# Performance work log

Hardware: AMD Instinct MI355X
Metric: run time of the kernel (lower is better)

## Reference

```python
import jax, jax.numpy as jnp
import numpy as np


def setup_inputs() -> dict:
    key = jax.random.key(0)
    ks = jax.random.split(key, 5)
    B, S, D, E, H = 8, 4096, 512, 4, 64
    x = jax.random.normal(ks[0], (B, S, D), dtype=jnp.float32)
    router_w = jax.random.normal(ks[1], (D, E), dtype=jnp.float32) * 0.02
    router_b = jnp.zeros((E,), dtype=jnp.float32)
    w1 = jax.random.normal(ks[2], (E, D, H), dtype=jnp.float32) * 0.02
    b1 = jnp.zeros((E, H), dtype=jnp.float32)
    w2 = jax.random.normal(ks[3], (E, H, D), dtype=jnp.float32) * 0.02
    b2 = jnp.zeros((E, D), dtype=jnp.float32)
    return {"x": x, "router_w": router_w, "router_b": router_b,
            "w1": w1, "b1": b1, "w2": w2, "b2": b2}


def reference(x, router_w, router_b, w1, b1, w2, b2):
    # Router: softmax over experts. weights: [B, S, E]
    weights = jax.nn.softmax(jnp.einsum('bsd,de->bse', x, router_w) + router_b, axis=-1)
    # All experts run densely on every token (batched over the E axis).
    # h: [B, S, E, H]; TF Dense(activation='gelu') uses exact (non-tanh) gelu.
    h = jax.nn.gelu(jnp.einsum('bsd,edh->bseh', x, w1) + b1, approximate=False)
    # expert outputs: [B, S, E, D]; Dropout is identity at inference.
    expert_out = jnp.einsum('bseh,ehd->bsed', h, w2) + b2
    # weighted sum over experts -> [B, S, D]
    return jnp.sum(expert_out * weights[..., None], axis=2)
```

## Files before the change

kernel.cpp:

```cpp
#include <hip/hip_runtime.h>
#include <hip/hip_bf16.h>
#include <math.h>


typedef short v8s __attribute__((ext_vector_type(8)));
typedef float v4f __attribute__((ext_vector_type(4)));

#define XS 520
#define HS 296

__device__ __forceinline__ unsigned short f2bf(float f) {
    unsigned int u = __builtin_bit_cast(unsigned int, f);
    u += 0x7fffu + ((u >> 16) & 1u);
    return (unsigned short)(u >> 16);
}

__global__ void moe_prep(const float* __restrict__ w1,
                         const float* __restrict__ w2,
                         const float* __restrict__ b2,
                         const float* __restrict__ rw,
                         unsigned short* __restrict__ w1p,
                         unsigned short* __restrict__ w2p,
                         unsigned short* __restrict__ rp) {
    int idx = blockIdx.x * 256 + threadIdx.x;
    if (idx < 131072) {
        int block = idx >> 9, within = idx & 511;
        int kb = block >> 4, cb = block & 15;
        int n = within >> 5, kl = within & 31;
        int k = kb * 32 + kl;
        int col = cb * 16 + n;
        int e = col >> 6, h = col & 63;
        w1p[idx] = f2bf(w1[(e * 512 + k) * 64 + h]);
    } else if (idx < 131072 + 147456) {
        int op = idx - 131072;
        int block = op >> 9, within = op & 511;
        int kb = block >> 5, cb = block & 31;
        int n = within >> 5, kl = within & 31;
        int k = kb * 32 + kl;
        int d = cb * 16 + n;
        float v = 0.f;
        if (k < 256) {
            int e = k >> 6, h = k & 63;
            v = w2[(e * 64 + h) * 512 + d];
        } else if (k < 260) {
            v = b2[(k - 256) * 512 + d];
        }
        w2p[op] = f2bf(v);
    } else if (idx < 131072 + 147456 + 8192) {
        int op = idx - (131072 + 147456);
        int kb = op >> 9, within = op & 511;
        int n = within >> 5, kl = within & 31;
        int k = kb * 32 + kl;
        float v = (n < 4) ? rw[k * 4 + n] : 0.f;
        rp[op] = f2bf(v);
    }
}

__global__ __launch_bounds__(512, 4)
void moe_main(const float* __restrict__ x,
              const float* __restrict__ rb,
              const float* __restrict__ b1,
              const unsigned short* __restrict__ w1p,
              const unsigned short* __restrict__ w2p,
              const unsigned short* __restrict__ rp,
              float* __restrict__ out) {
    __shared__ __align__(16) unsigned short lx[64 * XS];
    __shared__ float lw[64 * 4];

    const int tid  = threadIdx.x;
    const int lane = tid & 63, wv = tid >> 6;
    const int lr = lane & 15, lq = lane >> 4;
    const long t0 = (long)blockIdx.x * 64;

    const float4* xt = (const float4*)(x + t0 * 512);
    #pragma unroll
    for (int it = 0; it < 16; ++it) {
        int F = it * 512 + tid;
        int row = F >> 7, c4 = F & 127;
        float4 v = xt[F];
        unsigned int p0 = (unsigned int)f2bf(v.x) | ((unsigned int)f2bf(v.y) << 16);
        unsigned int p1 = (unsigned int)f2bf(v.z) | ((unsigned int)f2bf(v.w) << 16);
        *(uint2*)&lx[row * XS + c4 * 4] = make_uint2(p0, p1);
    }
    __syncthreads();

    v4f acc1[4][2];
    v4f accR;
    accR[0] = accR[1] = accR[2] = accR[3] = 0.f;
    #pragma unroll
    for (int mt = 0; mt < 4; ++mt)
        #pragma unroll
        for (int nt = 0; nt < 2; ++nt)
            acc1[mt][nt][0] = acc1[mt][nt][1] = acc1[mt][nt][2] = acc1[mt][nt][3] = 0.f;

    for (int kb = 0; kb < 16; ++kb) {
        v8s a[4], b[2];
        #pragma unroll
        for (int mt = 0; mt < 4; ++mt)
            a[mt] = *(const v8s*)(const void*)&lx[(16 * mt + lr) * XS + kb * 32 + lq * 8];
        #pragma unroll
        for (int nt = 0; nt < 2; ++nt)
            b[nt] = *(const v8s*)(const void*)&w1p[(size_t)(kb * 16 + 2 * wv + nt) * 512 + lr * 32 + lq * 8];
        if (wv < 4) {
            v8s ar = *(const v8s*)(const void*)&lx[(16 * wv + lr) * XS + kb * 32 + lq * 8];
            v8s br = *(const v8s*)(const void*)&rp[kb * 512 + lr * 32 + lq * 8];
            accR = __builtin_amdgcn_mfma_f32_16x16x32_bf16(ar, br, accR, 0, 0, 0);
        }
        #pragma unroll
        for (int mt = 0; mt < 4; ++mt)
            #pragma unroll
            for (int nt = 0; nt < 2; ++nt)
                acc1[mt][nt] = __builtin_amdgcn_mfma_f32_16x16x32_bf16(a[mt], b[nt], acc1[mt][nt], 0, 0, 0);
    }

    if (wv < 4) {
        float rbv = rb[lane & 3];
        #pragma unroll
        for (int r = 0; r < 4; ++r) {
            float v = accR[r] + rbv;
            float m = fmaxf(v, __shfl_xor(v, 1));
            m = fmaxf(m, __shfl_xor(m, 2));
            float e = expf(v - m);
            float s = e + __shfl_xor(e, 1);
            s += __shfl_xor(s, 2);
            if (lr < 4)
                lw[(16 * wv + lq * 4 + r) * 4 + lr] = e / s;
        }
    }

    __syncthreads();

    {
        const int e = wv >> 1;
        float b1v[2];
        #pragma unroll
        for (int nt = 0; nt < 2; ++nt)
            b1v[nt] = b1[e * 64 + 32 * (wv & 1) + 16 * nt + lr];
        #pragma unroll
        for (int mt = 0; mt < 4; ++mt) {
            #pragma unroll
            for (int r = 0; r < 4; ++r) {
                int row = 16 * mt + lq * 4 + r;
                float wt = lw[row * 4 + e];
                #pragma unroll
                for (int nt = 0; nt < 2; ++nt) {
                    float v = acc1[mt][nt][r] + b1v[nt];
                    float g = 0.5f * v * (1.f + erff(v * 0.70710678118f)) * wt;
                    lx[row * HS + 32 * wv + 16 * nt + lr] = f2bf(g);
                }
            }
        }
        if (tid < 256) {
            int r = tid >> 2, e4 = tid & 3;
            lx[r * HS + 256 + e4] = f2bf(lw[r * 4 + e4]);
            #pragma unroll
            for (int i = 0; i < 7; ++i)
                lx[r * HS + 260 + e4 + 4 * i] = 0;
        }
    }
    __syncthreads();

    v4f acc2[4][4];
    #pragma unroll
    for (int mt = 0; mt < 4; ++mt)
        #pragma unroll
        for (int nt = 0; nt < 4; ++nt)
            acc2[mt][nt][0] = acc2[mt][nt][1] = acc2[mt][nt][2] = acc2[mt][nt][3] = 0.f;

    for (int kb = 0; kb < 9; ++kb) {
        v8s a[4], b[4];
        #pragma unroll
        for (int mt = 0; mt < 4; ++mt)
            a[mt] = *(const v8s*)(const void*)&lx[(16 * mt + lr) * HS + kb * 32 + lq * 8];
        #pragma unroll
        for (int nt = 0; nt < 4; ++nt)
            b[nt] = *(const v8s*)(const void*)&w2p[(size_t)(kb * 32 + 4 * wv + nt) * 512 + lr * 32 + lq * 8];
        #pragma unroll
        for (int mt = 0; mt < 4; ++mt)
            #pragma unroll
            for (int nt = 0; nt < 4; ++nt)
                acc2[mt][nt] = __builtin_amdgcn_mfma_f32_16x16x32_bf16(a[mt], b[nt], acc2[mt][nt], 0, 0, 0);
    }

    float* ot = out + t0 * 512;
    #pragma unroll
    for (int mt = 0; mt < 4; ++mt)
        #pragma unroll
        for (int nt = 0; nt < 4; ++nt)
            #pragma unroll
            for (int r = 0; r < 4; ++r) {
                int row = 16 * mt + lq * 4 + r;
                int col = 64 * wv + 16 * nt + lr;
                ot[row * 512 + col] = acc2[mt][nt][r];
            }
}

extern "C" void kernel_launch(void* const* d_in, const int* in_sizes, int n_in,
                              void* d_out, int out_size, void* d_ws, size_t ws_size,
                              hipStream_t stream) {
    const float* x  = (const float*)d_in[0];
    const float* rw = (const float*)d_in[1];
    const float* rb = (const float*)d_in[2];
    const float* w1 = (const float*)d_in[3];
    const float* b1 = (const float*)d_in[4];
    const float* w2 = (const float*)d_in[5];
    const float* b2 = (const float*)d_in[6];

    unsigned short* w1p = (unsigned short*)d_ws;
    unsigned short* w2p = w1p + 131072;
    unsigned short* rp  = w2p + 147456;

    moe_prep<<<1120, 256, 0, stream>>>(w1, w2, b2, rw, w1p, w2p, rp);
    moe_main<<<512, 512, 0, stream>>>(x, rb, b1, w1p, w2p, rp, (float*)d_out);
}
```

Before: 156.5 us.

## Split fused MoE kernel into two GEMM kernels with global hidden buffer

Splits the single fused kernel into one kernel computing the router softmax and gated GELU hidden activations, which are written to a global bf16 buffer, and a second kernel doing the output GEMM over twice as many blocks. The first kernel now reads x straight from global memory into registers instead of staging it through LDS, and uses fewer threads per block with more accumulator tiles per wave. Exact erf and expf are replaced by a polynomial erf approximation and fast exp. This gives up fusion, adding an HBM round trip for the hidden buffer and an extra launch, in exchange for lower LDS use, higher occupancy and more parallelism in the second GEMM.

```diff
diff --git a/kernel.cpp b/kernel.cpp
--- a/kernel.cpp
+++ b/kernel.cpp
@@ -5,14 +5,24 @@
 
 typedef short v8s __attribute__((ext_vector_type(8)));
 typedef float v4f __attribute__((ext_vector_type(4)));
-
-#define XS 520
-#define HS 296
 
 __device__ __forceinline__ unsigned short f2bf(float f) {
     unsigned int u = __builtin_bit_cast(unsigned int, f);
     u += 0x7fffu + ((u >> 16) & 1u);
     return (unsigned short)(u >> 16);
+}
+__device__ __forceinline__ unsigned int pk2(float lo, float hi) {
+    return (unsigned int)f2bf(lo) | ((unsigned int)f2bf(hi) << 16);
+}
+__device__ __forceinline__ float gelu_fast(float v) {
+    float s  = v * 0.70710678118f;
+    float xa = fabsf(s);
+    float t  = 1.0f / (1.0f + 0.3275911f * xa);
+    float poly = t * (0.254829592f + t * (-0.284496736f + t * (1.421413741f +
+                 t * (-1.453152027f + t * 1.061405429f))));
+    float er = 1.0f - poly * __expf(-xa * xa);
+    er = copysignf(er, s);
+    return 0.5f * v * (1.0f + er);
 }
 
 __global__ void moe_prep(const float* __restrict__ w1,
@@ -56,15 +66,13 @@
     }
 }
 
-__global__ __launch_bounds__(512, 4)
-void moe_main(const float* __restrict__ x,
-              const float* __restrict__ rb,
-              const float* __restrict__ b1,
-              const unsigned short* __restrict__ w1p,
-              const unsigned short* __restrict__ w2p,
-              const unsigned short* __restrict__ rp,
-              float* __restrict__ out) {
-    __shared__ __align__(16) unsigned short lx[64 * XS];
+__global__ __launch_bounds__(256, 3)
+void moe_g1(const float* __restrict__ x,
+            const float* __restrict__ rb,
+            const float* __restrict__ b1,
+            const unsigned short* __restrict__ w1p,
+            const unsigned short* __restrict__ rp,
+            unsigned short* __restrict__ hbuf) {
     __shared__ float lw[64 * 4];
 
     const int tid  = threadIdx.x;
@@ -72,117 +80,114 @@
     const int lr = lane & 15, lq = lane >> 4;
     const long t0 = (long)blockIdx.x * 64;
 
-    const float4* xt = (const float4*)(x + t0 * 512);
-    #pragma unroll
-    for (int it = 0; it < 16; ++it) {
-        int F = it * 512 + tid;
-        int row = F >> 7, c4 = F & 127;
-        float4 v = xt[F];
-        unsigned int p0 = (unsigned int)f2bf(v.x) | ((unsigned int)f2bf(v.y) << 16);
-        unsigned int p1 = (unsigned int)f2bf(v.z) | ((unsigned int)f2bf(v.w) << 16);
-        *(uint2*)&lx[row * XS + c4 * 4] = make_uint2(p0, p1);
-    }
-    __syncthreads();
-
-    v4f acc1[4][2];
+    v4f acc1[4][4];
     v4f accR;
     accR[0] = accR[1] = accR[2] = accR[3] = 0.f;
     #pragma unroll
     for (int mt = 0; mt < 4; ++mt)
         #pragma unroll
-        for (int nt = 0; nt < 2; ++nt)
+        for (int nt = 0; nt < 4; ++nt)
             acc1[mt][nt][0] = acc1[mt][nt][1] = acc1[mt][nt][2] = acc1[mt][nt][3] = 0.f;
 
+    #pragma unroll 2
     for (int kb = 0; kb < 16; ++kb) {
-        v8s a[4], b[2];
+        v8s a[4], b[4];
+        #pragma unroll
+        for (int mt = 0; mt < 4; ++mt) {
+            const float4* p = (const float4*)(x + (size_t)(t0 + 16 * mt + lr) * 512 + kb * 32 + lq * 8);
+            float4 u0 = p[0], u1 = p[1];
+            uint4 c = make_uint4(pk2(u0.x, u0.y), pk2(u0.z, u0.w),
+                                 pk2(u1.x, u1.y), pk2(u1.z, u1.w));
+            a[mt] = __builtin_bit_cast(v8s, c);
+        }
+        #pragma unroll
+        for (int nt = 0; nt < 4; ++nt)
+            b[nt] = *(const v8s*)(const void*)&w1p[(size_t)(kb * 16 + wv * 4 + nt) * 512 + lr * 32 + lq * 8];
+        v8s br = *(const v8s*)(const void*)&rp[kb * 512 + lr * 32 + lq * 8];
+        accR = __builtin_amdgcn_mfma_f32_16x16x32_bf16(a[wv], br, accR, 0, 0, 0);
         #pragma unroll
         for (int mt = 0; mt < 4; ++mt)
-            a[mt] = *(const v8s*)(const void*)&lx[(16 * mt + lr) * XS + kb * 32 + lq * 8];
-        #pragma unroll
-        for (int nt = 0; nt < 2; ++nt)
-            b[nt] = *(const v8s*)(const void*)&w1p[(size_t)(kb * 16 + 2 * wv + nt) * 512 + lr * 32 + lq * 8];
-        if (wv < 4) {
-            v8s ar = *(const v8s*)(const void*)&lx[(16 * wv + lr) * XS + kb * 32 + lq * 8];
-            v8s br = *(const v8s*)(const void*)&rp[kb * 512 + lr * 32 + lq * 8];
-            accR = __builtin_amdgcn_mfma_f32_16x16x32_bf16(ar, br, accR, 0, 0, 0);
-        }
-        #pragma unroll
-        for (int mt = 0; mt < 4; ++mt)
-            #pragma unroll
-            for (int nt = 0; nt < 2; ++nt)
+            #pragma unroll
+            for (int nt = 0; nt < 4; ++nt)
                 acc1[mt][nt] = __builtin_amdgcn_mfma_f32_16x16x32_bf16(a[mt], b[nt], acc1[mt][nt], 0, 0, 0);
     }
 
-    if (wv < 4) {
+    {
         float rbv = rb[lane & 3];
         #pragma unroll
         for (int r = 0; r < 4; ++r) {
             float v = accR[r] + rbv;
             float m = fmaxf(v, __shfl_xor(v, 1));
             m = fmaxf(m, __shfl_xor(m, 2));
-            float e = expf(v - m);
+            float e = __expf(v - m);
             float s = e + __shfl_xor(e, 1);
             s += __shfl_xor(s, 2);
             if (lr < 4)
                 lw[(16 * wv + lq * 4 + r) * 4 + lr] = e / s;
         }
     }
-
     __syncthreads();
 
     {
-        const int e = wv >> 1;
-        float b1v[2];
-        #pragma unroll
-        for (int nt = 0; nt < 2; ++nt)
-            b1v[nt] = b1[e * 64 + 32 * (wv & 1) + 16 * nt + lr];
+        float b1v[4];
+        #pragma unroll
+        for (int nt = 0; nt < 4; ++nt) b1v[nt] = b1[wv * 64 + nt * 16 + lr];
         #pragma unroll
         for (int mt = 0; mt < 4; ++mt) {
             #pragma unroll
             for (int r = 0; r < 4; ++r) {
                 int row = 16 * mt + lq * 4 + r;
-                float wt = lw[row * 4 + e];
+                float wt = lw[row * 4 + wv];
                 #pragma unroll
-                for (int nt = 0; nt < 2; ++nt) {
+                for (int nt = 0; nt < 4; ++nt) {
                     float v = acc1[mt][nt][r] + b1v[nt];
-                    float g = 0.5f * v * (1.f + erff(v * 0.70710678118f)) * wt;
-                    lx[row * HS + 32 * wv + 16 * nt + lr] = f2bf(g);
+                    float g = gelu_fast(v) * wt;
+                    hbuf[(size_t)(t0 + row) * 288 + wv * 64 + nt * 16 + lr] = f2bf(g);
                 }
             }
         }
-        if (tid < 256) {
-            int r = tid >> 2, e4 = tid & 3;
-            lx[r * HS + 256 + e4] = f2bf(lw[r * 4 + e4]);
-            #pragma unroll
-            for (int i = 0; i < 7; ++i)
-                lx[r * HS + 260 + e4 + 4 * i] = 0;
-        }
-    }
-    __syncthreads();
-
-    v4f acc2[4][4];
+        int rr = tid >> 2, e4 = tid & 3;
+        hbuf[(size_t)(t0 + rr) * 288 + 256 + e4] = f2bf(lw[rr * 4 + e4]);
+        #pragma unroll
+        for (int i = 0; i < 7; ++i)
+            hbuf[(size_t)(t0 + rr) * 288 + 260 + e4 * 7 + i] = 0;
+    }
+}
+
+__global__ __launch_bounds__(256, 3)
+void moe_g2(const unsigned short* __restrict__ hbuf,
+            const unsigned short* __restrict__ w2p,
+            float* __restrict__ out) {
+    const int tid  = threadIdx.x;
+    const int lane = tid & 63, wv = tid >> 6;
+    const int lr = lane & 15, lq = lane >> 4;
+    const long t0 = (long)(blockIdx.x >> 1) * 64;
+    const int nh = blockIdx.x & 1;
+    const int cb0 = nh * 16 + wv * 4;
+
+    v4f acc[4][4];
     #pragma unroll
     for (int mt = 0; mt < 4; ++mt)
         #pragma unroll
         for (int nt = 0; nt < 4; ++nt)
-            acc2[mt][nt][0] = acc2[mt][nt][1] = acc2[mt][nt][2] = acc2[mt][nt][3] = 0.f;
-
+            acc[mt][nt][0] = acc[mt][nt][1] = acc[mt][nt][2] = acc[mt][nt][3] = 0.f;
+
+    #pragma unroll 3
     for (int kb = 0; kb < 9; ++kb) {
         v8s a[4], b[4];
         #pragma unroll
         for (int mt = 0; mt < 4; ++mt)
-            a[mt] = *(const v8s*)(const void*)&lx[(16 * mt + lr) * HS + kb * 32 + lq * 8];
-        #pragma unroll
-        for (int nt = 0; nt < 4; ++nt)
-            b[nt] = *(const v8s*)(const void*)&w2p[(size_t)(kb * 32 + 4 * wv + nt) * 512 + lr * 32 + lq * 8];
+            a[mt] = *(const v8s*)(const void*)&hbuf[(size_t)(t0 + 16 * mt + lr) * 288 + kb * 32 + lq * 8];
+        #pragma unroll
+        for (int nt = 0; nt < 4; ++nt)
+            b[nt] = *(const v8s*)(const void*)&w2p[(size_t)(kb * 32 + cb0 + nt) * 512 + lr * 32 + lq * 8];
         #pragma unroll
         for (int mt = 0; mt < 4; ++mt)
             #pragma unroll
             for (int nt = 0; nt < 4; ++nt)
-                acc2[mt][nt] = __builtin_amdgcn_mfma_f32_16x16x32_bf16(a[mt], b[nt], acc2[mt][nt], 0, 0, 0);
-    }
-
-    float* ot = out + t0 * 512;
+                acc[mt][nt] = __builtin_amdgcn_mfma_f32_16x16x32_bf16(a[mt], b[nt], acc[mt][nt], 0, 0, 0);
+    }
+
     #pragma unroll
     for (int mt = 0; mt < 4; ++mt)
         #pragma unroll
@@ -190,8 +195,8 @@
             #pragma unroll
             for (int r = 0; r < 4; ++r) {
                 int row = 16 * mt + lq * 4 + r;
-                int col = 64 * wv + 16 * nt + lr;
-                ot[row * 512 + col] = acc2[mt][nt][r];
+                int col = nh * 256 + wv * 64 + 16 * nt + lr;
+                out[(size_t)(t0 + row) * 512 + col] = acc[mt][nt][r];
             }
 }
 
@@ -206,10 +211,12 @@
     const float* w2 = (const float*)d_in[5];
     const float* b2 = (const float*)d_in[6];
 
-    unsigned short* w1p = (unsigned short*)d_ws;
-    unsigned short* w2p = w1p + 131072;
-    unsigned short* rp  = w2p + 147456;
+    unsigned short* w1p  = (unsigned short*)d_ws;
+    unsigned short* w2p  = w1p + 131072;
+    unsigned short* rp   = w2p + 147456;
+    unsigned short* hbuf = rp + 8192;
 
     moe_prep<<<1120, 256, 0, stream>>>(w1, w2, b2, rw, w1p, w2p, rp);
-    moe_main<<<512, 512, 0, stream>>>(x, rb, b1, w1p, w2p, rp, (float*)d_out);
-}
+    moe_g1<<<512, 256, 0, stream>>>(x, rb, b1, w1p, rp, hbuf);
+    moe_g2<<<1024, 256, 0, stream>>>(hbuf, w2p, (float*)d_out);
+}
```

Result: slower. 210.8 us (+34.7%).

## Halve block to 4 waves, double-buffer weight loads, use fast GELU

Applied to the files above, without the earlier changes.

Shrinks the block from 8 to 4 waves so each wave covers one expert's full 64-column hidden slice and two 64-column output halves. Weight fragments from global memory are now double-buffered so the next k-step's loads overlap the current MFMAs. Exact erff is replaced by an Abramowitz-Stegun erf polynomial with __expf, and softmax also uses __expf. The cost is more register pressure per wave and fewer waves per block to hide latency, plus a small accuracy loss in GELU.

```diff
diff --git a/kernel.cpp b/kernel.cpp
--- a/kernel.cpp
+++ b/kernel.cpp
@@ -13,6 +13,15 @@
     unsigned int u = __builtin_bit_cast(unsigned int, f);
     u += 0x7fffu + ((u >> 16) & 1u);
     return (unsigned short)(u >> 16);
+}
+__device__ __forceinline__ float gelu_fast(float v) {
+    float s  = v * 0.70710678118f;
+    float xa = fabsf(s);
+    float t  = 1.0f / (1.0f + 0.3275911f * xa);
+    float poly = t * (0.254829592f + t * (-0.284496736f + t * (1.421413741f +
+                 t * (-1.453152027f + t * 1.061405429f))));
+    float er = copysignf(1.0f - poly * __expf(-xa * xa), s);
+    return 0.5f * v * (1.0f + er);
 }
 
 __global__ void moe_prep(const float* __restrict__ w1,
@@ -56,7 +65,7 @@
     }
 }
 
-__global__ __launch_bounds__(512, 4)
+__global__ __launch_bounds__(256, 2)
 void moe_main(const float* __restrict__ x,
               const float* __restrict__ rb,
               const float* __restrict__ b1,
@@ -74,8 +83,8 @@
 
     const float4* xt = (const float4*)(x + t0 * 512);
     #pragma unroll
-    for (int it = 0; it < 16; ++it) {
-        int F = it * 512 + tid;
+    for (int it = 0; it < 32; ++it) {
+        int F = it * 256 + tid;
         int row = F >> 7, c4 = F & 127;
         float4 v = xt[F];
         unsigned int p0 = (unsigned int)f2bf(v.x) | ((unsigned int)f2bf(v.y) << 16);
@@ -84,115 +93,161 @@
     }
     __syncthreads();
 
-    v4f acc1[4][2];
+    v4f acc1[4][4];
     v4f accR;
     accR[0] = accR[1] = accR[2] = accR[3] = 0.f;
     #pragma unroll
     for (int mt = 0; mt < 4; ++mt)
         #pragma unroll
-        for (int nt = 0; nt < 2; ++nt)
+        for (int nt = 0; nt < 4; ++nt)
             acc1[mt][nt][0] = acc1[mt][nt][1] = acc1[mt][nt][2] = acc1[mt][nt][3] = 0.f;
 
-    for (int kb = 0; kb < 16; ++kb) {
-        v8s a[4], b[2];
-        #pragma unroll
-        for (int mt = 0; mt < 4; ++mt)
-            a[mt] = *(const v8s*)(const void*)&lx[(16 * mt + lr) * XS + kb * 32 + lq * 8];
-        #pragma unroll
-        for (int nt = 0; nt < 2; ++nt)
-            b[nt] = *(const v8s*)(const void*)&w1p[(size_t)(kb * 16 + 2 * wv + nt) * 512 + lr * 32 + lq * 8];
-        if (wv < 4) {
-            v8s ar = *(const v8s*)(const void*)&lx[(16 * wv + lr) * XS + kb * 32 + lq * 8];
-            v8s br = *(const v8s*)(const void*)&rp[kb * 512 + lr * 32 + lq * 8];
-            accR = __builtin_amdgcn_mfma_f32_16x16x32_bf16(ar, br, accR, 0, 0, 0);
-        }
-        #pragma unroll
-        for (int mt = 0; mt < 4; ++mt)
-            #pragma unroll
-            for (int nt = 0; nt < 2; ++nt)
-                acc1[mt][nt] = __builtin_amdgcn_mfma_f32_16x16x32_bf16(a[mt], b[nt], acc1[mt][nt], 0, 0, 0);
-    }
-
-    if (wv < 4) {
+    const unsigned short* w1base = w1p + (size_t)(wv * 4) * 512 + lr * 32 + lq * 8;
+    const unsigned short* rpbase = rp + lr * 32 + lq * 8;
+
+    #define LDW1(B, BR, kb) do {                                                   \
+        _Pragma("unroll")                                                          \
+        for (int nt_ = 0; nt_ < 4; ++nt_)                                          \
+            B[nt_] = *(const v8s*)(const void*)&w1base[(size_t)((kb) * 16 + nt_) * 512]; \
+        BR = *(const v8s*)(const void*)&rpbase[(kb) * 512];                        \
+    } while (0)
+
+    #define MM1(B, BR, kb) do {                                                    \
+        v8s a_[4];                                                                 \
+        _Pragma("unroll")                                                          \
+        for (int mt_ = 0; mt_ < 4; ++mt_)                                          \
+            a_[mt_] = *(const v8s*)(const void*)&lx[(16 * mt_ + lr) * XS + (kb) * 32 + lq * 8]; \
+        v8s ar_ = *(const v8s*)(const void*)&lx[(16 * wv + lr) * XS + (kb) * 32 + lq * 8];      \
+        accR = __builtin_amdgcn_mfma_f32_16x16x32_bf16(ar_, BR, accR, 0, 0, 0);    \
+        _Pragma("unroll")                                                          \
+        for (int mt_ = 0; mt_ < 4; ++mt_)                                          \
+            _Pragma("unroll")                                                      \
+            for (int nt_ = 0; nt_ < 4; ++nt_)                                      \
+                acc1[mt_][nt_] = __builtin_amdgcn_mfma_f32_16x16x32_bf16(a_[mt_], B[nt_], acc1[mt_][nt_], 0, 0, 0); \
+    } while (0)
+
+    {
+        v8s b0[4], b1[4], br0, br1;
+        LDW1(b0, br0, 0);
+        #pragma unroll
+        for (int kp = 0; kp < 8; ++kp) {
+            LDW1(b1, br1, 2 * kp + 1);
+            MM1(b0, br0, 2 * kp);
+            if (kp < 7) LDW1(b0, br0, 2 * kp + 2);
+            MM1(b1, br1, 2 * kp + 1);
+        }
+    }
+
+    {
         float rbv = rb[lane & 3];
         #pragma unroll
         for (int r = 0; r < 4; ++r) {
             float v = accR[r] + rbv;
             float m = fmaxf(v, __shfl_xor(v, 1));
             m = fmaxf(m, __shfl_xor(m, 2));
-            float e = expf(v - m);
+            float e = __expf(v - m);
             float s = e + __shfl_xor(e, 1);
             s += __shfl_xor(s, 2);
             if (lr < 4)
                 lw[(16 * wv + lq * 4 + r) * 4 + lr] = e / s;
         }
     }
-
     __syncthreads();
 
+    const unsigned short* w2base = w2p + (size_t)(wv * 8) * 512 + lr * 32 + lq * 8;
+
+    v8s c0[4], c1[4];
+    #pragma unroll
+    for (int nt_ = 0; nt_ < 4; ++nt_)
+        c0[nt_] = *(const v8s*)(const void*)&w2base[(size_t)nt_ * 512];
+
     {
-        const int e = wv >> 1;
-        float b1v[2];
-        #pragma unroll
-        for (int nt = 0; nt < 2; ++nt)
-            b1v[nt] = b1[e * 64 + 32 * (wv & 1) + 16 * nt + lr];
+        float b1v[4];
+        #pragma unroll
+        for (int nt = 0; nt < 4; ++nt) b1v[nt] = b1[wv * 64 + nt * 16 + lr];
         #pragma unroll
         for (int mt = 0; mt < 4; ++mt) {
             #pragma unroll
             for (int r = 0; r < 4; ++r) {
                 int row = 16 * mt + lq * 4 + r;
-                float wt = lw[row * 4 + e];
+                float wt = lw[row * 4 + wv];
                 #pragma unroll
-                for (int nt = 0; nt < 2; ++nt) {
+                for (int nt = 0; nt < 4; ++nt) {
                     float v = acc1[mt][nt][r] + b1v[nt];
-                    float g = 0.5f * v * (1.f + erff(v * 0.70710678118f)) * wt;
-                    lx[row * HS + 32 * wv + 16 * nt + lr] = f2bf(g);
+                    float g = gelu_fast(v) * wt;
+                    lx[row * HS + wv * 64 + nt * 16 + lr] = f2bf(g);
                 }
             }
         }
-        if (tid < 256) {
-            int r = tid >> 2, e4 = tid & 3;
-            lx[r * HS + 256 + e4] = f2bf(lw[r * 4 + e4]);
-            #pragma unroll
-            for (int i = 0; i < 7; ++i)
-                lx[r * HS + 260 + e4 + 4 * i] = 0;
-        }
+        int r = tid >> 2, e = tid & 3;
+        lx[r * HS + 256 + e] = f2bf(lw[tid]);
+        #pragma unroll
+        for (int i = 0; i < 7; ++i)
+            lx[r * HS + 260 + e + 4 * i] = 0;
     }
     __syncthreads();
 
-    v4f acc2[4][4];
-    #pragma unroll
-    for (int mt = 0; mt < 4; ++mt)
-        #pragma unroll
-        for (int nt = 0; nt < 4; ++nt)
-            acc2[mt][nt][0] = acc2[mt][nt][1] = acc2[mt][nt][2] = acc2[mt][nt][3] = 0.f;
-
-    for (int kb = 0; kb < 9; ++kb) {
-        v8s a[4], b[4];
+    float* ot = out + t0 * 512;
+
+    #define LDW2(C, kb, h) do {                                                    \
+        _Pragma("unroll")                                                          \
+        for (int nt_ = 0; nt_ < 4; ++nt_)                                          \
+            C[nt_] = *(const v8s*)(const void*)&w2base[(size_t)((kb) * 32 + (h) * 4 + nt_) * 512]; \
+    } while (0)
+
+    #define MM2(C, kb) do {                                                        \
+        v8s a_[4];                                                                 \
+        _Pragma("unroll")                                                          \
+        for (int mt_ = 0; mt_ < 4; ++mt_)                                          \
+            a_[mt_] = *(const v8s*)(const void*)&lx[(16 * mt_ + lr) * HS + (kb) * 32 + lq * 8]; \
+        _Pragma("unroll")                                                          \
+        for (int mt_ = 0; mt_ < 4; ++mt_)                                          \
+            _Pragma("unroll")                                                      \
+            for (int nt_ = 0; nt_ < 4; ++nt_)                                      \
+                acc2[mt_][nt_] = __builtin_amdgcn_mfma_f32_16x16x32_bf16(a_[mt_], C[nt_], acc2[mt_][nt_], 0, 0, 0); \
+    } while (0)
+
+    #pragma unroll 1
+    for (int half = 0; half < 2; ++half) {
+        v4f acc2[4][4];
         #pragma unroll
         for (int mt = 0; mt < 4; ++mt)
-            a[mt] = *(const v8s*)(const void*)&lx[(16 * mt + lr) * HS + kb * 32 + lq * 8];
-        #pragma unroll
-        for (int nt = 0; nt < 4; ++nt)
-            b[nt] = *(const v8s*)(const void*)&w2p[(size_t)(kb * 32 + 4 * wv + nt) * 512 + lr * 32 + lq * 8];
+            #pragma unroll
+            for (int nt = 0; nt < 4; ++nt)
+                acc2[mt][nt][0] = acc2[mt][nt][1] = acc2[mt][nt][2] = acc2[mt][nt][3] = 0.f;
+
+        #pragma unroll
+        for (int kp = 0; kp < 4; ++kp) {
+            LDW2(c1, 2 * kp + 1, half);
+            MM2(c0, 2 * kp);
+            LDW2(c0, 2 * kp + 2, half);
+            MM2(c1, 2 * kp + 1);
+        }
+        if (half == 0) {
+            LDW2(c1, 0, 1);
+        }
+        MM2(c0, 8);
+
         #pragma unroll
         for (int mt = 0; mt < 4; ++mt)
             #pragma unroll
             for (int nt = 0; nt < 4; ++nt)
-                acc2[mt][nt] = __builtin_amdgcn_mfma_f32_16x16x32_bf16(a[mt], b[nt], acc2[mt][nt], 0, 0, 0);
-    }
-
-    float* ot = out + t0 * 512;
-    #pragma unroll
-    for (int mt = 0; mt < 4; ++mt)
-        #pragma unroll
-        for (int nt = 0; nt < 4; ++nt)
-            #pragma unroll
-            for (int r = 0; r < 4; ++r) {
-                int row = 16 * mt + lq * 4 + r;
-                int col = 64 * wv + 16 * nt + lr;
-                ot[row * 512 + col] = acc2[mt][nt][r];
-            }
+                #pragma unroll
+                for (int r = 0; r < 4; ++r) {
+                    int row = 16 * mt + lq * 4 + r;
+                    int col = 128 * wv + 64 * half + 16 * nt + lr;
+                    ot[row * 512 + col] = acc2[mt][nt][r];
+                }
+
+        if (half == 0) {
+            #pragma unroll
+            for (int nt_ = 0; nt_ < 4; ++nt_) c0[nt_] = c1[nt_];
+        }
+    }
+    #undef LDW1
+    #undef MM1
+    #undef LDW2
+    #undef MM2
 }
 
 extern "C" void kernel_launch(void* const* d_in, const int* in_sizes, int n_in,
@@ -211,5 +266,5 @@
     unsigned short* rp  = w2p + 147456;
 
     moe_prep<<<1120, 256, 0, stream>>>(w1, w2, b2, rw, w1p, w2p, rp);
-    moe_main<<<512, 512, 0, stream>>>(x, rb, b1, w1p, w2p, rp, (float*)d_out);
-}
+    moe_main<<<512, 256, 0, stream>>>(x, rb, b1, w1p, w2p, rp, (float*)d_out);
+}
```

New measurement: 150.1 us. 4.1% less time.

## Switch to 32x32x16 MFMA tiles with 4-wave blocks and fast GELU

Applied to the files above, without the earlier changes.

Replaces the 16x16x32 bf16 MFMA with 32x32x16 MFMA and repacks the weights in the prep kernel to match the new fragment layout. The main kernel drops from 8 waves to 4 per block, so each wave computes a larger 64x64 or 64x128 tile, and the router GEMM now runs on two waves. Exact erff in GELU is replaced by the Abramowitz-Stegun polynomial with __expf, and expf becomes __expf. The intent is better MFMA throughput and fewer B-fragment loads per FLOP, at the cost of fewer waves per block for hiding latency and slightly lower GELU accuracy.

```diff
diff --git a/kernel.cpp b/kernel.cpp
--- a/kernel.cpp
+++ b/kernel.cpp
@@ -3,8 +3,8 @@
 #include <math.h>
 
 
-typedef short v8s __attribute__((ext_vector_type(8)));
-typedef float v4f __attribute__((ext_vector_type(4)));
+typedef short v8s  __attribute__((ext_vector_type(8)));
+typedef float v16f __attribute__((ext_vector_type(16)));
 
 #define XS 520
 #define HS 296
@@ -13,6 +13,15 @@
     unsigned int u = __builtin_bit_cast(unsigned int, f);
     u += 0x7fffu + ((u >> 16) & 1u);
     return (unsigned short)(u >> 16);
+}
+__device__ __forceinline__ float gelu_fast(float v) {
+    float s  = v * 0.70710678118f;
+    float xa = fabsf(s);
+    float t  = 1.0f / (1.0f + 0.3275911f * xa);
+    float poly = t * (0.254829592f + t * (-0.284496736f + t * (1.421413741f +
+                 t * (-1.453152027f + t * 1.061405429f))));
+    float er = copysignf(1.0f - poly * __expf(-xa * xa), s);
+    return 0.5f * v * (1.0f + er);
 }
 
 __global__ void moe_prep(const float* __restrict__ w1,
@@ -25,19 +34,19 @@
     int idx = blockIdx.x * 256 + threadIdx.x;
     if (idx < 131072) {
         int block = idx >> 9, within = idx & 511;
-        int kb = block >> 4, cb = block & 15;
-        int n = within >> 5, kl = within & 31;
-        int k = kb * 32 + kl;
-        int col = cb * 16 + n;
+        int kstep = block >> 3, cb = block & 7;
+        int n = within >> 4, kl = within & 15;
+        int k = kstep * 16 + kl;
+        int col = cb * 32 + n;
         int e = col >> 6, h = col & 63;
         w1p[idx] = f2bf(w1[(e * 512 + k) * 64 + h]);
     } else if (idx < 131072 + 147456) {
         int op = idx - 131072;
         int block = op >> 9, within = op & 511;
-        int kb = block >> 5, cb = block & 31;
-        int n = within >> 5, kl = within & 31;
-        int k = kb * 32 + kl;
-        int d = cb * 16 + n;
+        int kstep = block >> 4, cb = block & 15;
+        int n = within >> 4, kl = within & 15;
+        int k = kstep * 16 + kl;
+        int d = cb * 32 + n;
         float v = 0.f;
         if (k < 256) {
             int e = k >> 6, h = k & 63;
@@ -46,17 +55,17 @@
             v = b2[(k - 256) * 512 + d];
         }
         w2p[op] = f2bf(v);
-    } else if (idx < 131072 + 147456 + 8192) {
+    } else if (idx < 131072 + 147456 + 16384) {
         int op = idx - (131072 + 147456);
-        int kb = op >> 9, within = op & 511;
-        int n = within >> 5, kl = within & 31;
-        int k = kb * 32 + kl;
+        int kstep = op >> 9, within = op & 511;
+        int n = within >> 4, kl = within & 15;
+        int k = kstep * 16 + kl;
         float v = (n < 4) ? rw[k * 4 + n] : 0.f;
         rp[op] = f2bf(v);
     }
 }
 
-__global__ __launch_bounds__(512, 4)
+__global__ __launch_bounds__(256, 2)
 void moe_main(const float* __restrict__ x,
               const float* __restrict__ rb,
               const float* __restrict__ b1,
@@ -69,13 +78,13 @@
 
     const int tid  = threadIdx.x;
     const int lane = tid & 63, wv = tid >> 6;
-    const int lr = lane & 15, lq = lane >> 4;
+    const int ln = lane & 31, hi = lane >> 5;
     const long t0 = (long)blockIdx.x * 64;
 
     const float4* xt = (const float4*)(x + t0 * 512);
     #pragma unroll
-    for (int it = 0; it < 16; ++it) {
-        int F = it * 512 + tid;
+    for (int it = 0; it < 32; ++it) {
+        int F = it * 256 + tid;
         int row = F >> 7, c4 = F & 127;
         float4 v = xt[F];
         unsigned int p0 = (unsigned int)f2bf(v.x) | ((unsigned int)f2bf(v.y) << 16);
@@ -84,114 +93,114 @@
     }
     __syncthreads();
 
-    v4f acc1[4][2];
-    v4f accR;
-    accR[0] = accR[1] = accR[2] = accR[3] = 0.f;
-    #pragma unroll
-    for (int mt = 0; mt < 4; ++mt)
+    v16f acc1[2][2];
+    v16f accR;
+    #pragma unroll
+    for (int j = 0; j < 16; ++j) accR[j] = 0.f;
+    #pragma unroll
+    for (int mt = 0; mt < 2; ++mt)
         #pragma unroll
         for (int nt = 0; nt < 2; ++nt)
-            acc1[mt][nt][0] = acc1[mt][nt][1] = acc1[mt][nt][2] = acc1[mt][nt][3] = 0.f;
-
-    for (int kb = 0; kb < 16; ++kb) {
-        v8s a[4], b[2];
-        #pragma unroll
-        for (int mt = 0; mt < 4; ++mt)
-            a[mt] = *(const v8s*)(const void*)&lx[(16 * mt + lr) * XS + kb * 32 + lq * 8];
-        #pragma unroll
-        for (int nt = 0; nt < 2; ++nt)
-            b[nt] = *(const v8s*)(const void*)&w1p[(size_t)(kb * 16 + 2 * wv + nt) * 512 + lr * 32 + lq * 8];
-        if (wv < 4) {
-            v8s ar = *(const v8s*)(const void*)&lx[(16 * wv + lr) * XS + kb * 32 + lq * 8];
-            v8s br = *(const v8s*)(const void*)&rp[kb * 512 + lr * 32 + lq * 8];
-            accR = __builtin_amdgcn_mfma_f32_16x16x32_bf16(ar, br, accR, 0, 0, 0);
-        }
-        #pragma unroll
-        for (int mt = 0; mt < 4; ++mt)
-            #pragma unroll
-            for (int nt = 0; nt < 2; ++nt)
-                acc1[mt][nt] = __builtin_amdgcn_mfma_f32_16x16x32_bf16(a[mt], b[nt], acc1[mt][nt], 0, 0, 0);
-    }
-
-    if (wv < 4) {
-        float rbv = rb[lane & 3];
-        #pragma unroll
-        for (int r = 0; r < 4; ++r) {
-            float v = accR[r] + rbv;
+            #pragma unroll
+            for (int j = 0; j < 16; ++j) acc1[mt][nt][j] = 0.f;
+
+    const unsigned short* w1b = w1p + (size_t)(wv * 2) * 512 + ln * 16 + hi * 8;
+    const unsigned short* rpb = rp + ln * 16 + hi * 8;
+
+    for (int ks = 0; ks < 32; ++ks) {
+        v8s a0 = *(const v8s*)(const void*)&lx[ln * XS + ks * 16 + hi * 8];
+        v8s a1 = *(const v8s*)(const void*)&lx[(32 + ln) * XS + ks * 16 + hi * 8];
+        v8s b0 = *(const v8s*)(const void*)&w1b[(size_t)ks * 4096];
+        v8s b1f = *(const v8s*)(const void*)&w1b[(size_t)ks * 4096 + 512];
+        if (wv < 2) {
+            v8s br = *(const v8s*)(const void*)&rpb[ks * 512];
+            v8s ar = (wv == 0) ? a0 : a1;
+            accR = __builtin_amdgcn_mfma_f32_32x32x16_bf16(ar, br, accR, 0, 0, 0);
+        }
+        acc1[0][0] = __builtin_amdgcn_mfma_f32_32x32x16_bf16(a0, b0, acc1[0][0], 0, 0, 0);
+        acc1[0][1] = __builtin_amdgcn_mfma_f32_32x32x16_bf16(a0, b1f, acc1[0][1], 0, 0, 0);
+        acc1[1][0] = __builtin_amdgcn_mfma_f32_32x32x16_bf16(a1, b0, acc1[1][0], 0, 0, 0);
+        acc1[1][1] = __builtin_amdgcn_mfma_f32_32x32x16_bf16(a1, b1f, acc1[1][1], 0, 0, 0);
+    }
+
+    if (wv < 2) {
+        float rbv = rb[ln & 3];
+        #pragma unroll
+        for (int j = 0; j < 16; ++j) {
+            float v = accR[j] + rbv;
             float m = fmaxf(v, __shfl_xor(v, 1));
             m = fmaxf(m, __shfl_xor(m, 2));
-            float e = expf(v - m);
+            float e = __expf(v - m);
             float s = e + __shfl_xor(e, 1);
             s += __shfl_xor(s, 2);
-            if (lr < 4)
-                lw[(16 * wv + lq * 4 + r) * 4 + lr] = e / s;
-        }
-    }
-
+            if (ln < 4) {
+                int row = 32 * wv + (j & 3) + 8 * (j >> 2) + 4 * hi;
+                lw[row * 4 + ln] = e / s;
+            }
+        }
+    }
     __syncthreads();
 
     {
-        const int e = wv >> 1;
         float b1v[2];
         #pragma unroll
-        for (int nt = 0; nt < 2; ++nt)
-            b1v[nt] = b1[e * 64 + 32 * (wv & 1) + 16 * nt + lr];
-        #pragma unroll
-        for (int mt = 0; mt < 4; ++mt) {
-            #pragma unroll
-            for (int r = 0; r < 4; ++r) {
-                int row = 16 * mt + lq * 4 + r;
-                float wt = lw[row * 4 + e];
+        for (int nt = 0; nt < 2; ++nt) b1v[nt] = b1[wv * 64 + 32 * nt + ln];
+        #pragma unroll
+        for (int mt = 0; mt < 2; ++mt) {
+            #pragma unroll
+            for (int j = 0; j < 16; ++j) {
+                int row = 32 * mt + (j & 3) + 8 * (j >> 2) + 4 * hi;
+                float wt = lw[row * 4 + wv];
                 #pragma unroll
                 for (int nt = 0; nt < 2; ++nt) {
-                    float v = acc1[mt][nt][r] + b1v[nt];
-                    float g = 0.5f * v * (1.f + erff(v * 0.70710678118f)) * wt;
-                    lx[row * HS + 32 * wv + 16 * nt + lr] = f2bf(g);
+                    float v = acc1[mt][nt][j] + b1v[nt];
+                    float g = gelu_fast(v) * wt;
+                    lx[row * HS + wv * 64 + 32 * nt + ln] = f2bf(g);
                 }
             }
         }
-        if (tid < 256) {
-            int r = tid >> 2, e4 = tid & 3;
-            lx[r * HS + 256 + e4] = f2bf(lw[r * 4 + e4]);
-            #pragma unroll
-            for (int i = 0; i < 7; ++i)
-                lx[r * HS + 260 + e4 + 4 * i] = 0;
-        }
+        int r = tid >> 2, e = tid & 3;
+        lx[r * HS + 256 + e] = f2bf(lw[tid]);
+        #pragma unroll
+        for (int i = 0; i < 7; ++i)
+            lx[r * HS + 260 + e + 4 * i] = 0;
     }
     __syncthreads();
 
-    v4f acc2[4][4];
-    #pragma unroll
-    for (int mt = 0; mt < 4; ++mt)
+    v16f acc2[2][4];
+    #pragma unroll
+    for (int mt = 0; mt < 2; ++mt)
         #pragma unroll
         for (int nt = 0; nt < 4; ++nt)
-            acc2[mt][nt][0] = acc2[mt][nt][1] = acc2[mt][nt][2] = acc2[mt][nt][3] = 0.f;
-
-    for (int kb = 0; kb < 9; ++kb) {
-        v8s a[4], b[4];
-        #pragma unroll
-        for (int mt = 0; mt < 4; ++mt)
-            a[mt] = *(const v8s*)(const void*)&lx[(16 * mt + lr) * HS + kb * 32 + lq * 8];
+            #pragma unroll
+            for (int j = 0; j < 16; ++j) acc2[mt][nt][j] = 0.f;
+
+    const unsigned short* w2b = w2p + (size_t)(wv * 4) * 512 + ln * 16 + hi * 8;
+
+    for (int ks = 0; ks < 18; ++ks) {
+        v8s a0 = *(const v8s*)(const void*)&lx[ln * HS + ks * 16 + hi * 8];
+        v8s a1 = *(const v8s*)(const void*)&lx[(32 + ln) * HS + ks * 16 + hi * 8];
+        v8s b[4];
         #pragma unroll
         for (int nt = 0; nt < 4; ++nt)
-            b[nt] = *(const v8s*)(const void*)&w2p[(size_t)(kb * 32 + 4 * wv + nt) * 512 + lr * 32 + lq * 8];
-        #pragma unroll
-        for (int mt = 0; mt < 4; ++mt)
-            #pragma unroll
-            for (int nt = 0; nt < 4; ++nt)
-                acc2[mt][nt] = __builtin_amdgcn_mfma_f32_16x16x32_bf16(a[mt], b[nt], acc2[mt][nt], 0, 0, 0);
+            b[nt] = *(const v8s*)(const void*)&w2b[(size_t)ks * 8192 + nt * 512];
+        #pragma unroll
+        for (int nt = 0; nt < 4; ++nt) {
+            acc2[0][nt] = __builtin_amdgcn_mfma_f32_32x32x16_bf16(a0, b[nt], acc2[0][nt], 0, 0, 0);
+            acc2[1][nt] = __builtin_amdgcn_mfma_f32_32x32x16_bf16(a1, b[nt], acc2[1][nt], 0, 0, 0);
+        }
     }
 
     float* ot = out + t0 * 512;
     #pragma unroll
-    for (int mt = 0; mt < 4; ++mt)
+    for (int mt = 0; mt < 2; ++mt)
         #pragma unroll
         for (int nt = 0; nt < 4; ++nt)
             #pragma unroll
-            for (int r = 0; r < 4; ++r) {
-                int row = 16 * mt + lq * 4 + r;
-                int col = 64 * wv + 16 * nt + lr;
-                ot[row * 512 + col] = acc2[mt][nt][r];
+            for (int j = 0; j < 16; ++j) {
+                int row = 32 * mt + (j & 3) + 8 * (j >> 2) + 4 * hi;
+                int col = 128 * wv + 32 * nt + ln;
+                ot[row * 512 + col] = acc2[mt][nt][j];
             }
 }
 
@@ -210,6 +219,6 @@
     unsigned short* w2p = w1p + 131072;
     unsigned short* rp  = w2p + 147456;
 
-    moe_prep<<<1120, 256, 0, stream>>>(w1, w2, b2, rw, w1p, w2p, rp);
-    moe_main<<<512, 512, 0, stream>>>(x, rb, b1, w1p, w2p, rp, (float*)d_out);
-}
+    moe_prep<<<1152, 256, 0, stream>>>(w1, w2, b2, rw, w1p, w2p, rp);
+    moe_main<<<512, 256, 0, stream>>>(x, rb, b1, w1p, w2p, rp, (float*)d_out);
+}
```

Result: faster. 148.5 us (-5.1%).
